# Kernel tuning notes

Hardware: AMD Instinct MI355X
Metric: run time of the kernel (lower is better)

The kernel has to match this reference:

```python
import math
import jax, jax.numpy as jnp
import numpy as np

HID = 8
QNUM = 22
NUM_A = 11
NUM_LAYER = 6


def _ln(x, g, b, eps=1e-5):
    m = jnp.mean(x, axis=-1, keepdims=True)
    v = jnp.mean((x - m) ** 2, axis=-1, keepdims=True)
    return (x - m) / jnp.sqrt(v + eps) * g + b


def _conv1d_s2(x, w):
    # x: [N, C, L], w: [O, I, K=2], stride 2, no padding, no bias
    return jax.lax.conv_general_dilated(x, w, (2,), 'VALID', dimension_numbers=('NCH', 'OIH', 'NCH'))


def _qembed(hf):
    # product state amplitudes of RY(hf_q)|0> per qubit: [cos(t/2), sin(t/2)], kron over qubits
    c = jnp.cos(hf / 2.0)
    s = jnp.sin(hf / 2.0)
    state = jnp.ones((1,), dtype=hf.dtype)
    for q in range(hf.shape[0]):
        state = jnp.kron(state, jnp.stack([c[q], s[q]]))
    return state  # [2^Q]


def setup_inputs() -> dict:
    key = jax.random.key(0)
    ks = jax.random.split(key, 32)
    ix_list = [2] * NUM_A  # 2 electrons per atom -> n_e = 22 (even, <= QNUM)
    pos_ix = np.concatenate([np.arange(n) for n in ix_list])
    atom_ix = np.concatenate([np.full(n, i) for i, n in enumerate(ix_list)])
    L = NUM_LAYER
    g = lambda i, shp, s=1.0: jax.random.normal(ks[i], shp, dtype=jnp.float32) * s
    return dict(
        pos_a=g(0, (NUM_A, 3), 3.0),
        ix_a=jnp.asarray(ix_list, dtype=jnp.int32),
        pos_ix=jnp.asarray(pos_ix, dtype=jnp.int32),
        atom_ix=jnp.asarray(atom_ix, dtype=jnp.int32),
        rpos_w=g(1, (10, 3), 1.0),
        emb_w=g(2, (HID, 4), 0.5),
        emb_b=jnp.zeros((HID,), jnp.float32),
        Wq=g(3, (L, HID, HID), 0.35), bq=jnp.zeros((L, HID), jnp.float32),
        Wk=g(4, (L, HID, HID), 0.35), bk=jnp.zeros((L, HID), jnp.float32),
        Wv=g(5, (L, HID, HID), 0.35), bv=jnp.zeros((L, HID), jnp.float32),
        Wo=g(6, (L, HID, HID), 0.35), bo=jnp.zeros((L, HID), jnp.float32),
        W1=g(7, (L, 4 * HID, HID), 0.35), b1=jnp.zeros((L, 4 * HID), jnp.float32),
        W2=g(8, (L, HID, 4 * HID), 0.18), b2=jnp.zeros((L, HID), jnp.float32),
        ln1_g=jnp.ones((L, HID), jnp.float32), ln1_b=jnp.zeros((L, HID), jnp.float32),
        ln2_g=jnp.ones((L, HID), jnp.float32), ln2_b=jnp.zeros((L, HID), jnp.float32),
        Wi=g(9, (2 * HID, HID), 0.35), bi=jnp.zeros((2 * HID,), jnp.float32),
        ni_g=jnp.ones((2 * HID,), jnp.float32), ni_b=jnp.zeros((2 * HID,), jnp.float32),
        conv_a_w=g(10, (2 * HID, 2 * HID, 2), 0.25),
        conv_e_w=g(11, (2 * HID, 2 * HID, 2), 0.25),
        Wout=g(12, (2 ** QNUM, 2 * HID), 0.05),
        bout=jnp.zeros((2 ** QNUM,), jnp.float32),
    )


def reference(pos_a, ix_a, pos_ix, atom_ix, rpos_w, emb_w, emb_b,
              Wq, bq, Wk, bk, Wv, bv, Wo, bo, W1, b1, W2, b2,
              ln1_g, ln1_b, ln2_g, ln2_b,
              Wi, bi, ni_g, ni_b, conv_a_w, conv_e_w, Wout, bout):
    n_e = pos_ix.shape[0]
    pos_e = rpos_w[pos_ix] + pos_a[atom_ix]                 # [n_e, 3]
    ae = pos_e[:, None, :] - pos_a[None, :, :]              # [n_e, A, 3]
    r_ae = jnp.linalg.norm(ae, axis=2, keepdims=True)       # [n_e, A, 1]
    seq = jnp.concatenate([ae, r_ae], axis=-1) @ emb_w.T + emb_b  # [n_e, A, HID]
    amp_proto = ix_a.astype(seq.dtype)[None, :, None]       # broadcast of expanded ix_a
    amp_ae = jnp.std(r_ae, ddof=1)
    bias_ae = jnp.mean(r_ae)
    scale = jnp.sqrt(jnp.asarray(HID, seq.dtype))
    for l in range(Wq.shape[0]):
        x = amp_proto * seq
        q = x @ Wq[l].T + bq[l]
        k = x @ Wk[l].T + bk[l]
        v = x @ Wv[l].T + bv[l]
        att = jax.nn.softmax(jnp.einsum('bqh,bkh->bqk', q, k) / scale, axis=-1)
        a = jnp.einsum('bqk,bkh->bqh', att, v) @ Wo[l].T + bo[l]
        x = _ln(x + a, ln1_g[l], ln1_b[l])
        f = jax.nn.relu(x @ W1[l].T + b1[l]) @ W2[l].T + b2[l]
        seq = _ln(x + f, ln2_g[l], ln2_b[l])
    # pseudo-inverse projection (detached in torch)
    ae_inv = jax.lax.stop_gradient(jnp.linalg.inv(emb_w.T @ emb_w) @ emb_w.T)  # [4, HID]
    r = jnp.einsum('h,bah->ba', ae_inv[-1], seq)[..., None]  # [n_e, A, 1]
    r = amp_ae * (r - jnp.mean(r)) / jnp.std(r, ddof=1) + bias_ae
    x = (jnp.exp(-r) * amp_proto * seq) @ Wi.T + bi          # [n_e, A, 2*HID]
    x = jnp.swapaxes(x, -2, -1)                              # [n_e, 2*HID, A]
    y = jnp.mean(x, axis=-1)                                 # [n_e, 2*HID]
    amp_r = jnp.mean(jnp.exp(-jnp.swapaxes(r, -2, -1)), axis=-1)  # [n_e, 1]
    pad = jnp.zeros((x.shape[0], x.shape[1], 1), x.dtype)
    n_iter_a = (x.shape[-1] + 1) // 2
    for _ in range(n_iter_a):
        x = _conv1d_s2(jnp.concatenate([x, pad], axis=-1), conv_a_w)
    x = (amp_r * _ln(y + x[..., 0], ni_g, ni_b)).T           # [2*HID, n_e]
    y = jnp.mean(x, axis=-1)                                 # [2*HID]
    amp_r2 = jnp.mean(amp_r.T, axis=-1)                      # [1]
    x = x[None]                                              # [1, 2*HID, n_e]
    pad = jnp.zeros((1, x.shape[1], 1), x.dtype)
    n_iter_e = (x.shape[-1] + 1) // 2
    for _ in range(n_iter_e):
        x = _conv1d_s2(jnp.concatenate([x, pad], axis=-1), conv_e_w)
    x = amp_r2 * _ln(y + x[0, :, 0], ni_g, ni_b)             # [2*HID]
    psi = x @ Wout.T + bout                                  # [2^QNUM]
    hf = jnp.asarray(([math.pi, 0.0] * (n_e // 2)) + [0.0] * (QNUM - n_e), dtype=psi.dtype)
    bos = _qembed(hf)
    return psi + bos * (2.0 ** (QNUM / 2))
```

## Files before the change

### kernel.cpp

```cpp
#include <hip/hip_runtime.h>
#include <math.h>

#define NE 22
#define NA 11
#define HD 8
#define H2 16
#define QN 22
#define NL 6

struct QCS { float c[QN]; float s[QN]; };

__device__ __forceinline__ float block_reduce_sum(float v, float* red, int tid) {
  red[tid] = v;
  __syncthreads();
  for (int off = 128; off > 0; off >>= 1) {
    if (tid < off) red[tid] += red[tid + off];
    __syncthreads();
  }
  float s = red[0];
  __syncthreads();
  return s;
}

__device__ __forceinline__ void ln_vec(const float* x, int n, const float* g,
                                       const float* bb, float* o) {
  float m = 0.f;
  for (int i = 0; i < n; i++) m += x[i];
  m /= (float)n;
  float v = 0.f;
  for (int i = 0; i < n; i++) { float d = x[i] - m; v += d * d; }
  v /= (float)n;
  float is = 1.0f / sqrtf(v + 1e-5f);
  for (int i = 0; i < n; i++) o[i] = (x[i] - m) * is * g[i] + bb[i];
}

__global__ __launch_bounds__(256) void small_net_kernel(
    const float* __restrict__ pos_a, const int* __restrict__ ix_a,
    const int* __restrict__ pos_ix, const int* __restrict__ atom_ix,
    const float* __restrict__ rpos_w, const float* __restrict__ emb_w,
    const float* __restrict__ emb_b,
    const float* __restrict__ Wq, const float* __restrict__ bq,
    const float* __restrict__ Wk, const float* __restrict__ bk,
    const float* __restrict__ Wv, const float* __restrict__ bv,
    const float* __restrict__ Wo, const float* __restrict__ bo,
    const float* __restrict__ W1, const float* __restrict__ b1,
    const float* __restrict__ W2, const float* __restrict__ b2,
    const float* __restrict__ ln1_g, const float* __restrict__ ln1_b,
    const float* __restrict__ ln2_g, const float* __restrict__ ln2_b,
    const float* __restrict__ Wi, const float* __restrict__ bi,
    const float* __restrict__ ni_g, const float* __restrict__ ni_b,
    const float* __restrict__ conv_a_w, const float* __restrict__ conv_e_w,
    float* __restrict__ xf_out)
{
  const int tid = threadIdx.x;
  const int b = tid / NA;
  const int a = tid % NA;
  const bool act = (tid < NE * NA);

  __shared__ float s_pos_e[NE][3];
  __shared__ float s_amp[NA];
  __shared__ float s_seq[NE][NA][HD];
  __shared__ float s_x[NE][NA][HD];
  __shared__ float s_er[NE][NA];
  __shared__ float s_red[256];
  __shared__ float s_scal[8];
  __shared__ float s_aeinv[HD];
  __shared__ union {
    struct { float q[NE][NA][HD]; float k[NE][NA][HD]; float v[NE][NA][HD]; } att;
    struct { float A[NE * H2 * NA]; float B[NE * H2 * 6]; } conv;
  } u;
  __shared__ float s_y[NE][H2];
  __shared__ float s_ampr[NE];
  __shared__ float s_eA[H2 * NE];
  __shared__ float s_eB[H2 * NA];
  __shared__ float s_y2[H2];

  if (tid < NE) {
    int p = pos_ix[tid], am = atom_ix[tid];
    for (int j = 0; j < 3; j++) s_pos_e[tid][j] = rpos_w[p * 3 + j] + pos_a[am * 3 + j];
  }
  if (tid < NA) s_amp[tid] = (float)ix_a[tid];
  __syncthreads();

  float rae = 0.f;
  if (act) {
    float d0 = s_pos_e[b][0] - pos_a[a * 3 + 0];
    float d1 = s_pos_e[b][1] - pos_a[a * 3 + 1];
    float d2 = s_pos_e[b][2] - pos_a[a * 3 + 2];
    rae = sqrtf(d0 * d0 + d1 * d1 + d2 * d2);
    float in4[4] = { d0, d1, d2, rae };
    for (int h = 0; h < HD; h++) {
      float s = emb_b[h];
      for (int j = 0; j < 4; j++) s += in4[j] * emb_w[h * 4 + j];
      s_seq[b][a][h] = s;
    }
  }
  {
    float sum = block_reduce_sum(act ? rae : 0.f, s_red, tid);
    float mean = sum / (float)(NE * NA);
    float d = act ? (rae - mean) : 0.f;
    float ss = block_reduce_sum(d * d, s_red, tid);
    if (tid == 0) { s_scal[0] = sqrtf(ss / (float)(NE * NA - 1)); s_scal[1] = mean; }
  }
  __syncthreads();

  const float iscale = 1.0f / sqrtf((float)HD);
  for (int l = 0; l < NL; l++) {
    if (act) {
      float xv[HD];
      float amp = s_amp[a];
      for (int h = 0; h < HD; h++) { xv[h] = amp * s_seq[b][a][h]; s_x[b][a][h] = xv[h]; }
      for (int h = 0; h < HD; h++) {
        float qq = bq[l * HD + h], kk = bk[l * HD + h], vv = bv[l * HD + h];
        const float* wq = Wq + (size_t)(l * HD + h) * HD;
        const float* wk = Wk + (size_t)(l * HD + h) * HD;
        const float* wv = Wv + (size_t)(l * HD + h) * HD;
        for (int h2 = 0; h2 < HD; h2++) {
          qq += xv[h2] * wq[h2];
          kk += xv[h2] * wk[h2];
          vv += xv[h2] * wv[h2];
        }
        u.att.q[b][a][h] = qq; u.att.k[b][a][h] = kk; u.att.v[b][a][h] = vv;
      }
    }
    __syncthreads();
    if (act) {
      float sc[NA];
      float mx = -1e30f;
      for (int ka = 0; ka < NA; ka++) {
        float s = 0.f;
        for (int h = 0; h < HD; h++) s += u.att.q[b][a][h] * u.att.k[b][ka][h];
        s *= iscale;
        sc[ka] = s;
        mx = fmaxf(mx, s);
      }
      float den = 0.f;
      for (int ka = 0; ka < NA; ka++) { sc[ka] = expf(sc[ka] - mx); den += sc[ka]; }
      float inv_den = 1.0f / den;
      float av[HD];
      for (int h = 0; h < HD; h++) av[h] = 0.f;
      for (int ka = 0; ka < NA; ka++)
        for (int h = 0; h < HD; h++) av[h] += sc[ka] * u.att.v[b][ka][h];
      for (int h = 0; h < HD; h++) av[h] *= inv_den;
      float xr[HD], xn[HD];
      for (int h = 0; h < HD; h++) {
        float t = bo[l * HD + h];
        const float* wo = Wo + (size_t)(l * HD + h) * HD;
        for (int h2 = 0; h2 < HD; h2++) t += av[h2] * wo[h2];
        xr[h] = s_x[b][a][h] + t;
      }
      ln_vec(xr, HD, ln1_g + l * HD, ln1_b + l * HD, xn);
      float f2[HD];
      for (int h = 0; h < HD; h++) f2[h] = b2[l * HD + h];
      for (int o = 0; o < 4 * HD; o++) {
        float t = b1[l * 4 * HD + o];
        const float* w1 = W1 + (size_t)(l * 4 * HD + o) * HD;
        for (int h = 0; h < HD; h++) t += xn[h] * w1[h];
        t = fmaxf(t, 0.f);
        for (int h = 0; h < HD; h++) f2[h] += t * W2[(size_t)(l * HD + h) * (4 * HD) + o];
      }
      for (int h = 0; h < HD; h++) xr[h] = xn[h] + f2[h];
      ln_vec(xr, HD, ln2_g + l * HD, ln2_b + l * HD, xn);
      for (int h = 0; h < HD; h++) s_seq[b][a][h] = xn[h];
    }
    __syncthreads();
  }

  if (tid == 0) {
    double M[4][8];
    for (int i = 0; i < 4; i++)
      for (int j = 0; j < 4; j++) {
        double s = 0.0;
        for (int h = 0; h < HD; h++) s += (double)emb_w[h * 4 + i] * (double)emb_w[h * 4 + j];
        M[i][j] = s;
        M[i][4 + j] = (i == j) ? 1.0 : 0.0;
      }
    for (int c = 0; c < 4; c++) {
      int piv = c;
      for (int r2 = c + 1; r2 < 4; r2++) if (fabs(M[r2][c]) > fabs(M[piv][c])) piv = r2;
      if (piv != c) for (int j = 0; j < 8; j++) { double t = M[c][j]; M[c][j] = M[piv][j]; M[piv][j] = t; }
      double dd = M[c][c];
      for (int j = 0; j < 8; j++) M[c][j] /= dd;
      for (int r2 = 0; r2 < 4; r2++) if (r2 != c) {
        double f = M[r2][c];
        for (int j = 0; j < 8; j++) M[r2][j] -= f * M[c][j];
      }
    }
    for (int h = 0; h < HD; h++) {
      double s = 0.0;
      for (int j = 0; j < 4; j++) s += M[3][4 + j] * (double)emb_w[h * 4 + j];
      s_aeinv[h] = (float)s;
    }
  }
  __syncthreads();

  float rv = 0.f;
  if (act) for (int h = 0; h < HD; h++) rv += s_aeinv[h] * s_seq[b][a][h];
  {
    float sum = block_reduce_sum(act ? rv : 0.f, s_red, tid);
    float rm = sum / (float)(NE * NA);
    float d = act ? (rv - rm) : 0.f;
    float ss = block_reduce_sum(d * d, s_red, tid);
    float rs = sqrtf(ss / (float)(NE * NA - 1));
    if (act) {
      float rr = s_scal[0] * (rv - rm) / rs + s_scal[1];
      s_er[b][a] = expf(-rr);
    }
  }
  __syncthreads();

  if (act) {
    float e2 = s_er[b][a] * s_amp[a];
    float tv[HD];
    for (int h = 0; h < HD; h++) tv[h] = e2 * s_seq[b][a][h];
    for (int o = 0; o < H2; o++) {
      float s = bi[o];
      for (int h = 0; h < HD; h++) s += tv[h] * Wi[o * HD + h];
      u.conv.A[(b * H2 + o) * NA + a] = s;
    }
  }
  __syncthreads();

  for (int idx = tid; idx < NE * H2; idx += 256) {
    int bb = idx / H2, o = idx % H2;
    float s = 0.f;
    for (int a2 = 0; a2 < NA; a2++) s += u.conv.A[(bb * H2 + o) * NA + a2];
    s_y[bb][o] = s / (float)NA;
  }
  if (tid < NE) {
    float s = 0.f;
    for (int a2 = 0; a2 < NA; a2++) s += s_er[tid][a2];
    s_ampr[tid] = s / (float)NA;
  }
  __syncthreads();

  float* pin = u.conv.A;
  float* pout = u.conv.B;
  int L = NA;
  for (int it = 0; it < 6; it++) {
    int Lo = (L - 1) / 2 + 1;
    int total = NE * H2 * Lo;
    for (int idx = tid; idx < total; idx += 256) {
      int bb = idx / (H2 * Lo);
      int rem = idx - bb * (H2 * Lo);
      int o = rem / Lo;
      int j = rem - o * Lo;
      const float* base = pin + bb * H2 * L;
      float acc = 0.f;
      for (int i = 0; i < H2; i++) {
        float x0 = base[i * L + 2 * j];
        float x1 = (2 * j + 1 < L) ? base[i * L + 2 * j + 1] : 0.f;
        acc += x0 * conv_a_w[(o * H2 + i) * 2 + 0] + x1 * conv_a_w[(o * H2 + i) * 2 + 1];
      }
      pout[(bb * H2 + o) * Lo + j] = acc;
    }
    __syncthreads();
    float* t = pin; pin = pout; pout = t;
    L = Lo;
  }

  if (tid < NE) {
    float t[H2], oo[H2];
    for (int o = 0; o < H2; o++) t[o] = s_y[tid][o] + pin[tid * H2 + o];
    ln_vec(t, H2, ni_g, ni_b, oo);
    float ar = s_ampr[tid];
    for (int o = 0; o < H2; o++) s_eA[o * NE + tid] = ar * oo[o];
  }
  __syncthreads();
  if (tid < H2) {
    float s = 0.f;
    for (int bb = 0; bb < NE; bb++) s += s_eA[tid * NE + bb];
    s_y2[tid] = s / (float)NE;
  }
  if (tid == 0) {
    float s = 0.f;
    for (int bb = 0; bb < NE; bb++) s += s_ampr[bb];
    s_scal[4] = s / (float)NE;
  }
  __syncthreads();

  pin = s_eA; pout = s_eB;
  L = NE;
  for (int it = 0; it < 11; it++) {
    int Lo = (L - 1) / 2 + 1;
    int total = H2 * Lo;
    for (int idx = tid; idx < total; idx += 256) {
      int o = idx / Lo;
      int j = idx - o * Lo;
      float acc = 0.f;
      for (int i = 0; i < H2; i++) {
        float x0 = pin[i * L + 2 * j];
        float x1 = (2 * j + 1 < L) ? pin[i * L + 2 * j + 1] : 0.f;
        acc += x0 * conv_e_w[(o * H2 + i) * 2 + 0] + x1 * conv_e_w[(o * H2 + i) * 2 + 1];
      }
      pout[o * Lo + j] = acc;
    }
    __syncthreads();
    float* t = pin; pin = pout; pout = t;
    L = Lo;
  }

  if (tid == 0) {
    float t[H2], oo[H2];
    for (int o = 0; o < H2; o++) t[o] = s_y2[o] + pin[o];
    ln_vec(t, H2, ni_g, ni_b, oo);
    float a2 = s_scal[4];
    for (int o = 0; o < H2; o++) xf_out[o] = a2 * oo[o];
  }
}

__global__ __launch_bounds__(256) void psi_kernel(
    const float* __restrict__ Wout, const float* __restrict__ bout,
    const float* __restrict__ xf, float* __restrict__ out, QCS cs, int n)
{
  __shared__ float s_xf[H2];
  if (threadIdx.x < H2) s_xf[threadIdx.x] = xf[threadIdx.x];
  __syncthreads();
  int i = blockIdx.x * blockDim.x + threadIdx.x;
  if (i >= n) return;
  const float4* w4 = reinterpret_cast<const float4*>(Wout + (size_t)i * H2);
  float4 w0 = w4[0], w1 = w4[1], w2 = w4[2], w3 = w4[3];
  float acc = bout[i];
  acc += w0.x * s_xf[0]  + w0.y * s_xf[1]  + w0.z * s_xf[2]  + w0.w * s_xf[3];
  acc += w1.x * s_xf[4]  + w1.y * s_xf[5]  + w1.z * s_xf[6]  + w1.w * s_xf[7];
  acc += w2.x * s_xf[8]  + w2.y * s_xf[9]  + w2.z * s_xf[10] + w2.w * s_xf[11];
  acc += w3.x * s_xf[12] + w3.y * s_xf[13] + w3.z * s_xf[14] + w3.w * s_xf[15];
  unsigned int ii = (unsigned int)i;
  float p = (float)(1 << (QN / 2));
  #pragma unroll
  for (int q = 0; q < QN; q++) {
    p *= ((ii >> (QN - 1 - q)) & 1u) ? cs.s[q] : cs.c[q];
  }
  out[i] = acc + p;
}

extern "C" void kernel_launch(void* const* d_in, const int* in_sizes, int n_in,
                              void* d_out, int out_size, void* d_ws, size_t ws_size,
                              hipStream_t stream) {
  const float* pos_a   = (const float*)d_in[0];
  const int*   ix_a    = (const int*)d_in[1];
  const int*   pos_ix  = (const int*)d_in[2];
  const int*   atom_ix = (const int*)d_in[3];
  const float* rpos_w  = (const float*)d_in[4];
  const float* emb_w   = (const float*)d_in[5];
  const float* emb_b   = (const float*)d_in[6];
  const float* Wq = (const float*)d_in[7];   const float* bq = (const float*)d_in[8];
  const float* Wk = (const float*)d_in[9];   const float* bk = (const float*)d_in[10];
  const float* Wv = (const float*)d_in[11];  const float* bv = (const float*)d_in[12];
  const float* Wo = (const float*)d_in[13];  const float* bo = (const float*)d_in[14];
  const float* W1 = (const float*)d_in[15];  const float* b1 = (const float*)d_in[16];
  const float* W2 = (const float*)d_in[17];  const float* b2 = (const float*)d_in[18];
  const float* ln1_g = (const float*)d_in[19]; const float* ln1_b = (const float*)d_in[20];
  const float* ln2_g = (const float*)d_in[21]; const float* ln2_b = (const float*)d_in[22];
  const float* Wi = (const float*)d_in[23];  const float* bi = (const float*)d_in[24];
  const float* ni_g = (const float*)d_in[25]; const float* ni_b = (const float*)d_in[26];
  const float* conv_a_w = (const float*)d_in[27];
  const float* conv_e_w = (const float*)d_in[28];
  const float* Wout = (const float*)d_in[29];
  const float* bout = (const float*)d_in[30];
  float* xf = (float*)d_ws;

  small_net_kernel<<<1, 256, 0, stream>>>(pos_a, ix_a, pos_ix, atom_ix, rpos_w,
      emb_w, emb_b, Wq, bq, Wk, bk, Wv, bv, Wo, bo, W1, b1, W2, b2,
      ln1_g, ln1_b, ln2_g, ln2_b, Wi, bi, ni_g, ni_b, conv_a_w, conv_e_w, xf);

  QCS cs;
  int n_e = in_sizes[2];
  for (int q = 0; q < QN; q++) {
    float hf = (q < n_e && (q % 2 == 0)) ? (float)M_PI : 0.0f;
    cs.c[q] = cosf(0.5f * hf);
    cs.s[q] = sinf(0.5f * hf);
  }

  int n = out_size;
  int blocks = (n + 255) / 256;
  psi_kernel<<<blocks, 256, 0, stream>>>(Wout, bout, xf, (float*)d_out, cs, n);
}
```

Baseline: 580.5 us.

## Broadcast weights via readlane, repack conv layouts, coalesce Wout loads in psi

The small network kernel now loads each layer's weights once per wave into registers and broadcasts them with readlane instead of doing repeated global loads. Attention k/v buffers and the sequence use aligned float4 LDS accesses. The conv buffers are relaid out position-major with padding so each thread computes all 16 output channels for one position. The psi kernel reads Wout with coalesced float4 loads across lanes plus shuffle reductions, leaving only a quarter of the lanes to compute outputs. This adds register pressure and makes the psi stage's product loop run on fewer lanes.

New measurement: 504.3 us. 13.1% less time.

```diff
diff --git a/kernel.cpp b/kernel.cpp
--- a/kernel.cpp
+++ b/kernel.cpp
@@ -7,8 +7,12 @@
 #define H2 16
 #define QN 22
 #define NL 6
+#define CPAD 12
+#define CSTR 17
 
 struct QCS { float c[QN]; float s[QN]; };
+
+#define RL(v, l) __uint_as_float(__builtin_amdgcn_readlane(__float_as_uint(v), (l)))
 
 __device__ __forceinline__ float block_reduce_sum(float v, float* red, int tid) {
   red[tid] = v;
@@ -22,8 +26,8 @@
   return s;
 }
 
-__device__ __forceinline__ void ln_vec(const float* x, int n, const float* g,
-                                       const float* bb, float* o) {
+__device__ __forceinline__ void ln_vec(const float* x, int n, const float* __restrict__ g,
+                                       const float* __restrict__ bb, float* o) {
   float m = 0.f;
   for (int i = 0; i < n; i++) m += x[i];
   m /= (float)n;
@@ -53,27 +57,39 @@
     float* __restrict__ xf_out)
 {
   const int tid = threadIdx.x;
+  const int lane = tid & 63;
   const int b = tid / NA;
   const int a = tid % NA;
   const bool act = (tid < NE * NA);
 
+  __shared__ __align__(16) float s_seq[NE][NA][HD];
+  __shared__ __align__(16) float s_k[NE][NA][HD];
+  __shared__ __align__(16) float s_v[NE][NA][HD];
   __shared__ float s_pos_e[NE][3];
   __shared__ float s_amp[NA];
-  __shared__ float s_seq[NE][NA][HD];
-  __shared__ float s_x[NE][NA][HD];
   __shared__ float s_er[NE][NA];
   __shared__ float s_red[256];
   __shared__ float s_scal[8];
   __shared__ float s_aeinv[HD];
-  __shared__ union {
-    struct { float q[NE][NA][HD]; float k[NE][NA][HD]; float v[NE][NA][HD]; } att;
-    struct { float A[NE * H2 * NA]; float B[NE * H2 * 6]; } conv;
-  } u;
+  __shared__ float convA[NE * CPAD * CSTR];
+  __shared__ float convB[NE * CPAD * CSTR];
   __shared__ float s_y[NE][H2];
   __shared__ float s_ampr[NE];
-  __shared__ float s_eA[H2 * NE];
-  __shared__ float s_eB[H2 * NA];
+  __shared__ float s_eA[24 * CSTR];
+  __shared__ float s_eB[24 * CSTR];
   __shared__ float s_y2[H2];
+  __shared__ float s_cewt[32 * H2];
+
+  float cwr[8], wir[2];
+  #pragma unroll
+  for (int j = 0; j < 8; j++) cwr[j] = conv_a_w[j * 64 + lane];
+  #pragma unroll
+  for (int j = 0; j < 2; j++) wir[j] = Wi[j * 64 + lane];
+
+  for (int s = tid; s < 512; s += 256) {
+    int o = s >> 5, i = (s >> 1) & 15, k = s & 1;
+    s_cewt[(i * 2 + k) * 16 + o] = conv_e_w[s];
+  }
 
   if (tid < NE) {
     int p = pos_ix[tid], am = atom_ix[tid];
@@ -89,8 +105,10 @@
     float d2 = s_pos_e[b][2] - pos_a[a * 3 + 2];
     rae = sqrtf(d0 * d0 + d1 * d1 + d2 * d2);
     float in4[4] = { d0, d1, d2, rae };
+    #pragma unroll
     for (int h = 0; h < HD; h++) {
       float s = emb_b[h];
+      #pragma unroll
       for (int j = 0; j < 4; j++) s += in4[j] * emb_w[h * 4 + j];
       s_seq[b][a][h] = s;
     }
@@ -104,64 +122,99 @@
   }
   __syncthreads();
 
-  const float iscale = 1.0f / sqrtf((float)HD);
+  const float iscale = 0.35355339059327373f;
   for (int l = 0; l < NL; l++) {
+    float wr[12];
+    wr[0] = Wq[l * 64 + lane];
+    wr[1] = Wk[l * 64 + lane];
+    wr[2] = Wv[l * 64 + lane];
+    wr[3] = Wo[l * 64 + lane];
+    #pragma unroll
+    for (int j = 0; j < 4; j++) wr[4 + j] = W1[l * 256 + j * 64 + lane];
+    #pragma unroll
+    for (int j = 0; j < 4; j++) wr[8 + j] = W2[l * 256 + j * 64 + lane];
+
+    float xv[HD], qq[HD];
     if (act) {
-      float xv[HD];
       float amp = s_amp[a];
-      for (int h = 0; h < HD; h++) { xv[h] = amp * s_seq[b][a][h]; s_x[b][a][h] = xv[h]; }
+      float4 sq0 = *(const float4*)&s_seq[b][a][0];
+      float4 sq1 = *(const float4*)&s_seq[b][a][4];
+      xv[0] = amp * sq0.x; xv[1] = amp * sq0.y; xv[2] = amp * sq0.z; xv[3] = amp * sq0.w;
+      xv[4] = amp * sq1.x; xv[5] = amp * sq1.y; xv[6] = amp * sq1.z; xv[7] = amp * sq1.w;
+      float kk[HD], vv[HD];
+      #pragma unroll
       for (int h = 0; h < HD; h++) {
-        float qq = bq[l * HD + h], kk = bk[l * HD + h], vv = bv[l * HD + h];
-        const float* wq = Wq + (size_t)(l * HD + h) * HD;
-        const float* wk = Wk + (size_t)(l * HD + h) * HD;
-        const float* wv = Wv + (size_t)(l * HD + h) * HD;
+        float q_ = bq[l * HD + h], k_ = bk[l * HD + h], v_ = bv[l * HD + h];
+        #pragma unroll
         for (int h2 = 0; h2 < HD; h2++) {
-          qq += xv[h2] * wq[h2];
-          kk += xv[h2] * wk[h2];
-          vv += xv[h2] * wv[h2];
+          q_ += xv[h2] * RL(wr[0], h * 8 + h2);
+          k_ += xv[h2] * RL(wr[1], h * 8 + h2);
+          v_ += xv[h2] * RL(wr[2], h * 8 + h2);
         }
-        u.att.q[b][a][h] = qq; u.att.k[b][a][h] = kk; u.att.v[b][a][h] = vv;
-      }
+        qq[h] = q_; kk[h] = k_; vv[h] = v_;
+      }
+      *(float4*)&s_k[b][a][0] = make_float4(kk[0], kk[1], kk[2], kk[3]);
+      *(float4*)&s_k[b][a][4] = make_float4(kk[4], kk[5], kk[6], kk[7]);
+      *(float4*)&s_v[b][a][0] = make_float4(vv[0], vv[1], vv[2], vv[3]);
+      *(float4*)&s_v[b][a][4] = make_float4(vv[4], vv[5], vv[6], vv[7]);
     }
     __syncthreads();
     if (act) {
       float sc[NA];
       float mx = -1e30f;
+      #pragma unroll
       for (int ka = 0; ka < NA; ka++) {
-        float s = 0.f;
-        for (int h = 0; h < HD; h++) s += u.att.q[b][a][h] * u.att.k[b][ka][h];
+        float4 k0 = *(const float4*)&s_k[b][ka][0];
+        float4 k1 = *(const float4*)&s_k[b][ka][4];
+        float s = qq[0]*k0.x + qq[1]*k0.y + qq[2]*k0.z + qq[3]*k0.w
+                + qq[4]*k1.x + qq[5]*k1.y + qq[6]*k1.z + qq[7]*k1.w;
         s *= iscale;
         sc[ka] = s;
         mx = fmaxf(mx, s);
       }
       float den = 0.f;
+      #pragma unroll
       for (int ka = 0; ka < NA; ka++) { sc[ka] = expf(sc[ka] - mx); den += sc[ka]; }
       float inv_den = 1.0f / den;
       float av[HD];
+      #pragma unroll
       for (int h = 0; h < HD; h++) av[h] = 0.f;
-      for (int ka = 0; ka < NA; ka++)
-        for (int h = 0; h < HD; h++) av[h] += sc[ka] * u.att.v[b][ka][h];
+      #pragma unroll
+      for (int ka = 0; ka < NA; ka++) {
+        float4 v0 = *(const float4*)&s_v[b][ka][0];
+        float4 v1 = *(const float4*)&s_v[b][ka][4];
+        float p = sc[ka];
+        av[0] += p * v0.x; av[1] += p * v0.y; av[2] += p * v0.z; av[3] += p * v0.w;
+        av[4] += p * v1.x; av[5] += p * v1.y; av[6] += p * v1.z; av[7] += p * v1.w;
+      }
+      #pragma unroll
       for (int h = 0; h < HD; h++) av[h] *= inv_den;
       float xr[HD], xn[HD];
+      #pragma unroll
       for (int h = 0; h < HD; h++) {
         float t = bo[l * HD + h];
-        const float* wo = Wo + (size_t)(l * HD + h) * HD;
-        for (int h2 = 0; h2 < HD; h2++) t += av[h2] * wo[h2];
-        xr[h] = s_x[b][a][h] + t;
+        #pragma unroll
+        for (int h2 = 0; h2 < HD; h2++) t += av[h2] * RL(wr[3], h * 8 + h2);
+        xr[h] = xv[h] + t;
       }
       ln_vec(xr, HD, ln1_g + l * HD, ln1_b + l * HD, xn);
       float f2[HD];
+      #pragma unroll
       for (int h = 0; h < HD; h++) f2[h] = b2[l * HD + h];
-      for (int o = 0; o < 4 * HD; o++) {
-        float t = b1[l * 4 * HD + o];
-        const float* w1 = W1 + (size_t)(l * 4 * HD + o) * HD;
-        for (int h = 0; h < HD; h++) t += xn[h] * w1[h];
+      #pragma unroll
+      for (int o = 0; o < 32; o++) {
+        float t = b1[l * 32 + o];
+        #pragma unroll
+        for (int h = 0; h < HD; h++) t += xn[h] * RL(wr[4 + ((o * 8 + h) >> 6)], (o * 8 + h) & 63);
         t = fmaxf(t, 0.f);
-        for (int h = 0; h < HD; h++) f2[h] += t * W2[(size_t)(l * HD + h) * (4 * HD) + o];
-      }
+        #pragma unroll
+        for (int h = 0; h < HD; h++) f2[h] += t * RL(wr[8 + ((h * 32 + o) >> 6)], (h * 32 + o) & 63);
+      }
+      #pragma unroll
       for (int h = 0; h < HD; h++) xr[h] = xn[h] + f2[h];
       ln_vec(xr, HD, ln2_g + l * HD, ln2_b + l * HD, xn);
-      for (int h = 0; h < HD; h++) s_seq[b][a][h] = xn[h];
+      *(float4*)&s_seq[b][a][0] = make_float4(xn[0], xn[1], xn[2], xn[3]);
+      *(float4*)&s_seq[b][a][4] = make_float4(xn[4], xn[5], xn[6], xn[7]);
     }
     __syncthreads();
   }
@@ -195,7 +248,10 @@
   __syncthreads();
 
   float rv = 0.f;
-  if (act) for (int h = 0; h < HD; h++) rv += s_aeinv[h] * s_seq[b][a][h];
+  if (act) {
+    #pragma unroll
+    for (int h = 0; h < HD; h++) rv += s_aeinv[h] * s_seq[b][a][h];
+  }
   {
     float sum = block_reduce_sum(act ? rv : 0.f, s_red, tid);
     float rm = sum / (float)(NE * NA);
@@ -211,20 +267,26 @@
 
   if (act) {
     float e2 = s_er[b][a] * s_amp[a];
-    float tv[HD];
-    for (int h = 0; h < HD; h++) tv[h] = e2 * s_seq[b][a][h];
+    float4 sq0 = *(const float4*)&s_seq[b][a][0];
+    float4 sq1 = *(const float4*)&s_seq[b][a][4];
+    float tv[HD] = { e2*sq0.x, e2*sq0.y, e2*sq0.z, e2*sq0.w,
+                     e2*sq1.x, e2*sq1.y, e2*sq1.z, e2*sq1.w };
+    #pragma unroll
     for (int o = 0; o < H2; o++) {
       float s = bi[o];
-      for (int h = 0; h < HD; h++) s += tv[h] * Wi[o * HD + h];
-      u.conv.A[(b * H2 + o) * NA + a] = s;
-    }
-  }
+      #pragma unroll
+      for (int h = 0; h < HD; h++) s += tv[h] * RL(wir[(o * 8 + h) >> 6], (o * 8 + h) & 63);
+      convA[(b * CPAD + a) * CSTR + o] = s;
+    }
+  }
+  for (int z = tid; z < NE * H2; z += 256)
+    convA[((z >> 4) * CPAD + 11) * CSTR + (z & 15)] = 0.f;
   __syncthreads();
 
   for (int idx = tid; idx < NE * H2; idx += 256) {
-    int bb = idx / H2, o = idx % H2;
+    int bb = idx >> 4, o = idx & 15;
     float s = 0.f;
-    for (int a2 = 0; a2 < NA; a2++) s += u.conv.A[(bb * H2 + o) * NA + a2];
+    for (int a2 = 0; a2 < NA; a2++) s += convA[(bb * CPAD + a2) * CSTR + o];
     s_y[bb][o] = s / (float)NA;
   }
   if (tid < NE) {
@@ -234,26 +296,32 @@
   }
   __syncthreads();
 
-  float* pin = u.conv.A;
-  float* pout = u.conv.B;
+  float* pin = convA;
+  float* pout = convB;
   int L = NA;
   for (int it = 0; it < 6; it++) {
     int Lo = (L - 1) / 2 + 1;
-    int total = NE * H2 * Lo;
-    for (int idx = tid; idx < total; idx += 256) {
-      int bb = idx / (H2 * Lo);
-      int rem = idx - bb * (H2 * Lo);
-      int o = rem / Lo;
-      int j = rem - o * Lo;
-      const float* base = pin + bb * H2 * L;
-      float acc = 0.f;
-      for (int i = 0; i < H2; i++) {
-        float x0 = base[i * L + 2 * j];
-        float x1 = (2 * j + 1 < L) ? base[i * L + 2 * j + 1] : 0.f;
-        acc += x0 * conv_a_w[(o * H2 + i) * 2 + 0] + x1 * conv_a_w[(o * H2 + i) * 2 + 1];
-      }
-      pout[(bb * H2 + o) * Lo + j] = acc;
-    }
+    for (int pos = tid; pos < NE * Lo; pos += 256) {
+      int bb = pos / Lo, j = pos - bb * Lo;
+      const float* r0 = pin + (bb * CPAD + 2 * j) * CSTR;
+      const float* r1 = r0 + CSTR;
+      float x0[16], x1[16];
+      #pragma unroll
+      for (int i = 0; i < 16; i++) { x0[i] = r0[i]; x1[i] = r1[i]; }
+      float* wrow = pout + (bb * CPAD + j) * CSTR;
+      #pragma unroll
+      for (int o = 0; o < 16; o++) {
+        float acc = 0.f;
+        #pragma unroll
+        for (int i = 0; i < 16; i++) {
+          acc += x0[i] * RL(cwr[((o * 16 + i) * 2) >> 6], ((o * 16 + i) * 2) & 63)
+               + x1[i] * RL(cwr[((o * 16 + i) * 2 + 1) >> 6], ((o * 16 + i) * 2 + 1) & 63);
+        }
+        wrow[o] = acc;
+      }
+    }
+    for (int z = tid; z < NE * H2; z += 256)
+      pout[((z >> 4) * CPAD + Lo) * CSTR + (z & 15)] = 0.f;
     __syncthreads();
     float* t = pin; pin = pout; pout = t;
     L = Lo;
@@ -261,15 +329,18 @@
 
   if (tid < NE) {
     float t[H2], oo[H2];
-    for (int o = 0; o < H2; o++) t[o] = s_y[tid][o] + pin[tid * H2 + o];
+    #pragma unroll
+    for (int o = 0; o < H2; o++) t[o] = s_y[tid][o] + pin[(tid * CPAD) * CSTR + o];
     ln_vec(t, H2, ni_g, ni_b, oo);
     float ar = s_ampr[tid];
-    for (int o = 0; o < H2; o++) s_eA[o * NE + tid] = ar * oo[o];
-  }
+    #pragma unroll
+    for (int o = 0; o < H2; o++) s_eA[tid * CSTR + o] = ar * oo[o];
+  }
+  if (tid < H2) s_eA[NE * CSTR + tid] = 0.f;
   __syncthreads();
   if (tid < H2) {
     float s = 0.f;
-    for (int bb = 0; bb < NE; bb++) s += s_eA[tid * NE + bb];
+    for (int bb = 0; bb < NE; bb++) s += s_eA[bb * CSTR + tid];
     s_y2[tid] = s / (float)NE;
   }
   if (tid == 0) {
@@ -279,30 +350,30 @@
   }
   __syncthreads();
 
-  pin = s_eA; pout = s_eB;
+  float* pinE = s_eA;
+  float* poutE = s_eB;
   L = NE;
   for (int it = 0; it < 11; it++) {
     int Lo = (L - 1) / 2 + 1;
-    int total = H2 * Lo;
-    for (int idx = tid; idx < total; idx += 256) {
-      int o = idx / Lo;
-      int j = idx - o * Lo;
+    for (int idx = tid; idx < Lo * H2; idx += 256) {
+      int j = idx >> 4, o = idx & 15;
+      const float* r0 = pinE + (2 * j) * CSTR;
+      const float* r1 = r0 + CSTR;
       float acc = 0.f;
-      for (int i = 0; i < H2; i++) {
-        float x0 = pin[i * L + 2 * j];
-        float x1 = (2 * j + 1 < L) ? pin[i * L + 2 * j + 1] : 0.f;
-        acc += x0 * conv_e_w[(o * H2 + i) * 2 + 0] + x1 * conv_e_w[(o * H2 + i) * 2 + 1];
-      }
-      pout[o * Lo + j] = acc;
-    }
+      #pragma unroll
+      for (int i = 0; i < 16; i++)
+        acc += r0[i] * s_cewt[(i * 2) * 16 + o] + r1[i] * s_cewt[(i * 2 + 1) * 16 + o];
+      poutE[j * CSTR + o] = acc;
+    }
+    if (tid < H2) poutE[Lo * CSTR + tid] = 0.f;
     __syncthreads();
-    float* t = pin; pin = pout; pout = t;
+    float* t = pinE; pinE = poutE; poutE = t;
     L = Lo;
   }
 
   if (tid == 0) {
     float t[H2], oo[H2];
-    for (int o = 0; o < H2; o++) t[o] = s_y2[o] + pin[o];
+    for (int o = 0; o < H2; o++) t[o] = s_y2[o] + pinE[o];
     ln_vec(t, H2, ni_g, ni_b, oo);
     float a2 = s_scal[4];
     for (int o = 0; o < H2; o++) xf_out[o] = a2 * oo[o];
@@ -316,22 +387,29 @@
   __shared__ float s_xf[H2];
   if (threadIdx.x < H2) s_xf[threadIdx.x] = xf[threadIdx.x];
   __syncthreads();
-  int i = blockIdx.x * blockDim.x + threadIdx.x;
-  if (i >= n) return;
-  const float4* w4 = reinterpret_cast<const float4*>(Wout + (size_t)i * H2);
-  float4 w0 = w4[0], w1 = w4[1], w2 = w4[2], w3 = w4[3];
-  float acc = bout[i];
-  acc += w0.x * s_xf[0]  + w0.y * s_xf[1]  + w0.z * s_xf[2]  + w0.w * s_xf[3];
-  acc += w1.x * s_xf[4]  + w1.y * s_xf[5]  + w1.z * s_xf[6]  + w1.w * s_xf[7];
-  acc += w2.x * s_xf[8]  + w2.y * s_xf[9]  + w2.z * s_xf[10] + w2.w * s_xf[11];
-  acc += w3.x * s_xf[12] + w3.y * s_xf[13] + w3.z * s_xf[14] + w3.w * s_xf[15];
-  unsigned int ii = (unsigned int)i;
-  float p = (float)(1 << (QN / 2));
+  int lane = threadIdx.x & 63;
+  int waveBase = blockIdx.x * 256 + (threadIdx.x & ~63);
+  if (waveBase >= n) return;
+  const float4* W4 = (const float4*)Wout + (size_t)waveBase * 4;
+  int q = lane & 3;
+  float4 xq = make_float4(s_xf[q * 4], s_xf[q * 4 + 1], s_xf[q * 4 + 2], s_xf[q * 4 + 3]);
   #pragma unroll
-  for (int q = 0; q < QN; q++) {
-    p *= ((ii >> (QN - 1 - q)) & 1u) ? cs.s[q] : cs.c[q];
-  }
-  out[i] = acc + p;
+  for (int j = 0; j < 4; j++) {
+    float4 w = W4[j * 64 + lane];
+    float p = w.x * xq.x + w.y * xq.y + w.z * xq.z + w.w * xq.w;
+    p += __shfl_xor(p, 1, 64);
+    p += __shfl_xor(p, 2, 64);
+    if (q == 0) {
+      int row = waveBase + j * 16 + (lane >> 2);
+      float acc = bout[row] + p;
+      unsigned int ii = (unsigned int)row;
+      float pr = (float)(1 << (QN / 2));
+      #pragma unroll
+      for (int qb = 0; qb < QN; qb++)
+        pr *= ((ii >> (QN - 1 - qb)) & 1u) ? cs.s[qb] : cs.c[qb];
+      out[row] = acc + pr;
+    }
+  }
 }
 
 extern "C" void kernel_launch(void* const* d_in, const int* in_sizes, int n_in,
```
